# Kernel tuning notes

Hardware: AMD Instinct MI355X
Metric: run time of the kernel (lower is better)

Reference implementation:

```python
import jax, jax.numpy as jnp
import numpy as np

DIM = 1024
NUM_HEADS = 16
HEAD_DIM = DIM // NUM_HEADS
HIDDEN = 2 * DIM  # swiglu hidden


def rotate_half(x):
    x1, x2 = jnp.split(x, 2, axis=-1)
    return jnp.concatenate((-x2, x1), axis=-1)


def setup_inputs() -> dict:
    key = jax.random.key(0)
    ks = jax.random.split(key, 9)
    s = lambda fan_in: 1.0 / np.sqrt(fan_in)
    x = jax.random.normal(ks[0], (4, 2048, DIM), dtype=jnp.float32)
    qkv_w = jax.random.uniform(ks[1], (3 * DIM, DIM), minval=-s(DIM), maxval=s(DIM))
    proj_w = jax.random.uniform(ks[2], (DIM, DIM), minval=-s(DIM), maxval=s(DIM))
    proj_b = jax.random.uniform(ks[3], (DIM,), minval=-s(DIM), maxval=s(DIM))
    w1_w = jax.random.uniform(ks[4], (HIDDEN, DIM), minval=-s(DIM), maxval=s(DIM))
    w1_b = jnp.zeros((HIDDEN,), jnp.float32)
    w2_w = jax.random.uniform(ks[5], (HIDDEN, DIM), minval=-s(DIM), maxval=s(DIM))
    w2_b = jnp.zeros((HIDDEN,), jnp.float32)
    w3_w = jax.random.uniform(ks[6], (DIM, HIDDEN), minval=-s(HIDDEN), maxval=s(HIDDEN))
    w3_b = jnp.zeros((DIM,), jnp.float32)
    return {"x": x, "qkv_w": qkv_w, "proj_w": proj_w, "proj_b": proj_b,
            "w1_w": w1_w, "w1_b": w1_b, "w2_w": w2_w, "w2_b": w2_b,
            "w3_w": w3_w, "w3_b": w3_b}


def reference(x, qkv_w, proj_w, proj_b, w1_w, w1_b, w2_w, w2_b, w3_w, w3_b):
    B, N, C = x.shape
    H, D = NUM_HEADS, HEAD_DIM
    scale = D ** -0.5
    # QKV projection (no bias)
    qkv = jnp.einsum('bnc,fc->bnf', x, qkv_w).reshape(B, N, 3, H, D)
    qkv = jnp.transpose(qkv, (2, 0, 3, 1, 4))  # [3, B, H, N, D]
    q, k, v = qkv[0], qkv[1], qkv[2]
    # Rotary embeddings
    inv_freq = 1.0 / (10000.0 ** (jnp.arange(0, D, 2, dtype=jnp.float32) / D))
    t = jnp.arange(N, dtype=jnp.float32)
    freqs = jnp.einsum('i,j->ij', t, inv_freq)
    emb = jnp.concatenate((freqs, freqs), axis=-1)[None, None]  # [1,1,N,D]
    cos, sin = jnp.cos(emb), jnp.sin(emb)
    q = q * cos + rotate_half(q) * sin
    k = k * cos + rotate_half(k) * sin
    # Attention (non-causal, as in source)
    attn = jnp.einsum('bhnd,bhmd->bhnm', q, k) * scale
    attn = jax.nn.softmax(attn, axis=-1)
    out = jnp.einsum('bhnm,bhmd->bhnd', attn, v)
    out = jnp.transpose(out, (0, 2, 1, 3)).reshape(B, N, C)
    out = jnp.einsum('bnc,fc->bnf', out, proj_w) + proj_b
    # SwiGLU MLP
    x1 = jnp.einsum('bnc,fc->bnf', out, w1_w) + w1_b
    x2 = jnp.einsum('bnc,fc->bnf', out, w2_w) + w2_b
    hidden = jax.nn.silu(x1) * x2
    return jnp.einsum('bnh,fh->bnf', hidden, w3_w) + w3_b
```

## Files before the change

### kernel.cpp

```cpp
#include <hip/hip_runtime.h>
#include <hip/hip_bf16.h>
#include <math.h>


#define SEQ     2048
#define BATCH   4
#define NH      16
#define CDIM    1024
#define MROWS   8192

typedef __bf16 bf16x8 __attribute__((ext_vector_type(8)));
typedef float  floatx4 __attribute__((ext_vector_type(4)));
typedef float  floatx16 __attribute__((ext_vector_type(16)));
typedef unsigned int u32;

__device__ __forceinline__ unsigned short f2bf(float f) {
    __bf16 h = (__bf16)f;
    return __builtin_bit_cast(unsigned short, h);
}
__device__ __forceinline__ float fexp2(float x) {
    float r; asm("v_exp_f32 %0, %1" : "=v"(r) : "v"(x)); return r;
}
__device__ __forceinline__ float frcp(float x) {
    float r; asm("v_rcp_f32 %0, %1" : "=v"(r) : "v"(x)); return r;
}
__device__ __forceinline__ u32 cvtpk(float lo, float hi) {
    u32 w; asm("v_cvt_pk_bf16_f32 %0, %1, %2" : "=v"(w) : "v"(lo), "v"(hi));
    return w;
}
__device__ __forceinline__ floatx4 mfma16(bf16x8 a, bf16x8 b, floatx4 c) {
    return __builtin_amdgcn_mfma_f32_16x16x32_bf16(a, b, c, 0, 0, 0);
}
__device__ __forceinline__ floatx16 mfma32(bf16x8 a, bf16x8 b, floatx16 c) {
    return __builtin_amdgcn_mfma_f32_32x32x16_bf16(a, b, c, 0, 0, 0);
}
__device__ __forceinline__ void gld16(void* lds, const void* g) {
    __builtin_amdgcn_global_load_lds(
        (const __attribute__((address_space(1))) u32*)g,
        (__attribute__((address_space(3))) u32*)lds, 16, 0, 0);
}
__device__ __forceinline__ void wait_vm0_barrier() {
    asm volatile("s_waitcnt vmcnt(0)" ::: "memory");
    __builtin_amdgcn_s_barrier();
    __builtin_amdgcn_sched_barrier(0);
}
__device__ __forceinline__ void raw_barrier() {
    __builtin_amdgcn_s_barrier();
    __builtin_amdgcn_sched_barrier(0);
}

template <int OUTMODE, bool BIAS>
__global__ __launch_bounds__(256) void mgemm(
    const unsigned short* __restrict__ A,
    const unsigned short* __restrict__ B,
    const float* __restrict__ bias,
    void* __restrict__ C, int ldc,
    int K)
{
    __shared__ __align__(16) unsigned short As[2][128 * 32];
    __shared__ __align__(16) unsigned short Bs[2][128 * 32];

    const int tid  = threadIdx.x;
    const int lane = tid & 63;
    const int wave = tid >> 6;
    const int l16  = lane & 15;
    const int quad = lane >> 4;
    const int wm = (wave >> 1) * 64, wn = (wave & 1) * 64;
    const int bm = blockIdx.y, bn = blockIdx.x;

    const unsigned short* Ag = A + (size_t)(bm * 128) * K;
    const unsigned short* Bg = B + (size_t)(bn * 128) * K;

    const int srow0 = wave * 32 + (lane >> 2);
    const int scol  = 8 * ((lane & 3) ^ ((lane >> 3) & 3));
    const unsigned short* gA0 = Ag + (size_t)srow0 * K + scol;
    const unsigned short* gA1 = Ag + (size_t)(srow0 + 16) * K + scol;
    const unsigned short* gB0 = Bg + (size_t)srow0 * K + scol;
    const unsigned short* gB1 = Bg + (size_t)(srow0 + 16) * K + scol;

    auto stage = [&](int b, int kt) {
        gld16(&As[b][(wave * 2 + 0) * 512], gA0 + kt);
        gld16(&As[b][(wave * 2 + 1) * 512], gA1 + kt);
        gld16(&Bs[b][(wave * 2 + 0) * 512], gB0 + kt);
        gld16(&Bs[b][(wave * 2 + 1) * 512], gB1 + kt);
    };

    const int qsw = (quad ^ ((l16 >> 1) & 3)) * 8;

    floatx4 acc[4][4] = {};
    const int NK = K >> 5;

    stage(0, 0);
    wait_vm0_barrier();

    for (int i = 0; i < NK; ++i) {
        const int cur = i & 1;
        if (i + 1 < NK) stage(cur ^ 1, (i + 1) * 32);

        bf16x8 af[4], bfr[4];
        #pragma unroll
        for (int mt = 0; mt < 4; ++mt)
            af[mt] = *(const bf16x8*)&As[cur][(wm + mt * 16 + l16) * 32 + qsw];
        #pragma unroll
        for (int nt = 0; nt < 4; ++nt)
            bfr[nt] = *(const bf16x8*)&Bs[cur][(wn + nt * 16 + l16) * 32 + qsw];
        #pragma unroll
        for (int mt = 0; mt < 4; ++mt)
            #pragma unroll
            for (int nt = 0; nt < 4; ++nt)
                acc[mt][nt] = mfma16(af[mt], bfr[nt], acc[mt][nt]);

        if (i + 1 < NK) wait_vm0_barrier();
        else            raw_barrier();
    }

    #pragma unroll
    for (int nt = 0; nt < 4; ++nt) {
        const int gcol = bn * 128 + wn + nt * 16 + l16;
        const float bv = BIAS ? bias[gcol] : 0.0f;
        #pragma unroll
        for (int mt = 0; mt < 4; ++mt) {
            #pragma unroll
            for (int r = 0; r < 4; ++r) {
                const int grow = bm * 128 + wm + mt * 16 + quad * 4 + r;
                float v = acc[mt][nt][r] + bv;
                if (OUTMODE == 0)
                    ((float*)C)[(size_t)grow * ldc + gcol] = v;
                else
                    ((unsigned short*)C)[(size_t)grow * ldc + gcol] = f2bf(v);
            }
        }
    }
}

__global__ __launch_bounds__(256) void mgemm_glu(
    const unsigned short* __restrict__ A,
    const unsigned short* __restrict__ B1,
    const unsigned short* __restrict__ B2,
    const float* __restrict__ bias1,
    const float* __restrict__ bias2,
    unsigned short* __restrict__ C, int ldc,
    int K)
{
    __shared__ __align__(16) unsigned short As[2][128 * 32];
    __shared__ __align__(16) unsigned short B1s[2][64 * 32];
    __shared__ __align__(16) unsigned short B2s[2][64 * 32];

    const int tid  = threadIdx.x;
    const int lane = tid & 63;
    const int wave = tid >> 6;
    const int l16  = lane & 15;
    const int quad = lane >> 4;
    const int wm = (wave >> 1) * 64, wn = (wave & 1) * 32;
    const int bm = blockIdx.y, bn = blockIdx.x;

    const unsigned short* Ag  = A  + (size_t)(bm * 128) * K;
    const unsigned short* B1g = B1 + (size_t)(bn * 64) * K;
    const unsigned short* B2g = B2 + (size_t)(bn * 64) * K;

    const int arow = wave * 32 + (lane >> 2);
    const int brow = wave * 16 + (lane >> 2);
    const int scol = 8 * ((lane & 3) ^ ((lane >> 3) & 3));
    const unsigned short* gA0 = Ag  + (size_t)arow * K + scol;
    const unsigned short* gA1 = Ag  + (size_t)(arow + 16) * K + scol;
    const unsigned short* gB1 = B1g + (size_t)brow * K + scol;
    const unsigned short* gB2 = B2g + (size_t)brow * K + scol;

    auto stage = [&](int b, int kt) {
        gld16(&As[b][(wave * 2 + 0) * 512], gA0 + kt);
        gld16(&As[b][(wave * 2 + 1) * 512], gA1 + kt);
        gld16(&B1s[b][wave * 512], gB1 + kt);
        gld16(&B2s[b][wave * 512], gB2 + kt);
    };

    const int qsw = (quad ^ ((l16 >> 1) & 3)) * 8;

    floatx4 acc1[4][2] = {};
    floatx4 acc2[4][2] = {};
    const int NK = K >> 5;

    stage(0, 0);
    wait_vm0_barrier();

    for (int i = 0; i < NK; ++i) {
        const int cur = i & 1;
        if (i + 1 < NK) stage(cur ^ 1, (i + 1) * 32);

        bf16x8 af[4], b1f[2], b2f[2];
        #pragma unroll
        for (int mt = 0; mt < 4; ++mt)
            af[mt] = *(const bf16x8*)&As[cur][(wm + mt * 16 + l16) * 32 + qsw];
        #pragma unroll
        for (int nt = 0; nt < 2; ++nt) {
            b1f[nt] = *(const bf16x8*)&B1s[cur][(wn + nt * 16 + l16) * 32 + qsw];
            b2f[nt] = *(const bf16x8*)&B2s[cur][(wn + nt * 16 + l16) * 32 + qsw];
        }
        #pragma unroll
        for (int mt = 0; mt < 4; ++mt)
            #pragma unroll
            for (int nt = 0; nt < 2; ++nt) {
                acc1[mt][nt] = mfma16(af[mt], b1f[nt], acc1[mt][nt]);
                acc2[mt][nt] = mfma16(af[mt], b2f[nt], acc2[mt][nt]);
            }

        if (i + 1 < NK) wait_vm0_barrier();
        else            raw_barrier();
    }

    #pragma unroll
    for (int nt = 0; nt < 2; ++nt) {
        const int gcol = bn * 64 + wn + nt * 16 + l16;
        const float b1 = bias1[gcol];
        const float b2 = bias2[gcol];
        #pragma unroll
        for (int mt = 0; mt < 4; ++mt) {
            #pragma unroll
            for (int r = 0; r < 4; ++r) {
                const int grow = bm * 128 + wm + mt * 16 + quad * 4 + r;
                const float x1 = acc1[mt][nt][r] + b1;
                const float x2 = acc2[mt][nt][r] + b2;
                const float e = fexp2(x1 * -1.44269504088896f);
                const float v = x1 * frcp(1.0f + e) * x2;
                C[(size_t)grow * ldc + gcol] = f2bf(v);
            }
        }
    }
}

__global__ __launch_bounds__(256) void mgemm_qkv(
    const unsigned short* __restrict__ A,
    const unsigned short* __restrict__ B,
    const float* __restrict__ tab,
    unsigned short* __restrict__ Qb,
    unsigned short* __restrict__ Kb,
    unsigned short* __restrict__ Vtb)
{
    __shared__ __align__(16) unsigned short As[2][128 * 32];
    __shared__ __align__(16) unsigned short Bs[2][128 * 32];

    const int tid  = threadIdx.x;
    const int lane = tid & 63;
    const int wave = tid >> 6;
    const int l16  = lane & 15;
    const int quad = lane >> 4;
    const int wm = (wave >> 1) * 64, wn = (wave & 1) * 64;
    const int bm = blockIdx.y, bn = blockIdx.x;
    const int K = CDIM;

    const unsigned short* Ag = A + (size_t)(bm * 128) * K;
    const unsigned short* Bg = B + (size_t)(bn * 128) * K;

    const int srow0 = wave * 32 + (lane >> 2);
    const int scol  = 8 * ((lane & 3) ^ ((lane >> 3) & 3));
    const unsigned short* gA0 = Ag + (size_t)srow0 * K + scol;
    const unsigned short* gA1 = Ag + (size_t)(srow0 + 16) * K + scol;
    const unsigned short* gB0 = Bg + (size_t)srow0 * K + scol;
    const unsigned short* gB1 = Bg + (size_t)(srow0 + 16) * K + scol;

    auto stage = [&](int b, int kt) {
        gld16(&As[b][(wave * 2 + 0) * 512], gA0 + kt);
        gld16(&As[b][(wave * 2 + 1) * 512], gA1 + kt);
        gld16(&Bs[b][(wave * 2 + 0) * 512], gB0 + kt);
        gld16(&Bs[b][(wave * 2 + 1) * 512], gB1 + kt);
    };

    const int qsw = (quad ^ ((l16 >> 1) & 3)) * 8;

    floatx4 acc[4][4] = {};
    const int NK = K >> 5;

    stage(0, 0);
    wait_vm0_barrier();

    for (int i = 0; i < NK; ++i) {
        const int cur = i & 1;
        if (i + 1 < NK) stage(cur ^ 1, (i + 1) * 32);

        bf16x8 af[4], bfr[4];
        #pragma unroll
        for (int mt = 0; mt < 4; ++mt)
            af[mt] = *(const bf16x8*)&As[cur][(wm + mt * 16 + l16) * 32 + qsw];
        #pragma unroll
        for (int nt = 0; nt < 4; ++nt)
            bfr[nt] = *(const bf16x8*)&Bs[cur][(wn + nt * 16 + l16) * 32 + qsw];
        #pragma unroll
        for (int mt = 0; mt < 4; ++mt)
            #pragma unroll
            for (int nt = 0; nt < 4; ++nt)
                acc[mt][nt] = mfma16(af[mt], bfr[nt], acc[mt][nt]);

        if (i + 1 < NK) wait_vm0_barrier();
        else            raw_barrier();
    }

    const int colbase0 = bn * 128;
    const int part = colbase0 >> 10;

    if (part == 2) {
        unsigned short* T = &As[0][0];
        #pragma unroll
        for (int mt = 0; mt < 4; ++mt) {
            __syncthreads();
            #pragma unroll
            for (int nt = 0; nt < 4; ++nt) {
                ushort4 pk;
                pk.x = f2bf(acc[mt][nt][0]); pk.y = f2bf(acc[mt][nt][1]);
                pk.z = f2bf(acc[mt][nt][2]); pk.w = f2bf(acc[mt][nt][3]);
                *(ushort4*)&T[((wave * 64 + nt * 16 + l16) * 16) + quad * 4] = pk;
            }
            __syncthreads();
            const int w2 = tid >> 6, d = tid & 63;
            const int nrow0 = bm * 128 + (w2 >> 1) * 64 + mt * 16;
            const int b = nrow0 >> 11, n0 = nrow0 & 2047;
            const int h2 = ((bn * 128 + (w2 & 1) * 64) & 1023) >> 6;
            unsigned short* dst = Vtb +
                ((size_t)(b * NH + h2) * 64 + d) * 2048 + n0;
            const int tb = (w2 * 64 + d) * 16;
            *(uint4*)dst       = *(const uint4*)&T[tb];
            *(uint4*)(dst + 8) = *(const uint4*)&T[tb + 8];
        }
    } else {
        const float qscale = (part == 0) ? 0.125f * 1.44269504088896f : 1.0f;
        const int h = ((colbase0 + wn) & 1023) >> 6;
        #pragma unroll
        for (int mt = 0; mt < 4; ++mt) {
            #pragma unroll
            for (int r = 0; r < 4; ++r) {
                const int grow = bm * 128 + wm + mt * 16 + quad * 4 + r;
                const int b = grow >> 11, n = grow & 2047;
                unsigned short* dst =
                    (part == 0 ? Qb : Kb) + ((size_t)(b * NH + h) * 2048 + n) * 64;
                #pragma unroll
                for (int nt = 0; nt < 2; ++nt) {
                    const int i = nt * 16 + l16;
                    const float c  = tab[(n * 32 + i) * 2];
                    const float sn = tab[(n * 32 + i) * 2 + 1];
                    const float x1 = acc[mt][nt][r];
                    const float x2v = acc[mt][nt + 2][r];
                    dst[i]      = f2bf((x1 * c - x2v * sn) * qscale);
                    dst[i + 32] = f2bf((x2v * c + x1 * sn) * qscale);
                }
            }
        }
    }
}

__global__ __launch_bounds__(256) void attn_mfma(
    const unsigned short* __restrict__ Qb,
    const unsigned short* __restrict__ Kb,
    const unsigned short* __restrict__ Vtb,
    unsigned short* __restrict__ Ob)
{
    const int bh = blockIdx.x;
    const int qt = blockIdx.y;
    const int tid = threadIdx.x;
    const int lane = tid & 63, wave = tid >> 6;
    const int r32 = lane & 31, hi = lane >> 5;
    const int qrow = wave * 32 + r32;

    __shared__ unsigned short QP[128][72];
    __shared__ unsigned short Ks[64][72];
    __shared__ unsigned short Vs[64][72];

    const unsigned short* Qg = Qb + ((size_t)bh * 2048 + qt * 128) * 64;
    const unsigned short* Kg = Kb + (size_t)bh * 2048 * 64;
    const unsigned short* Vg = Vtb + (size_t)bh * 64 * 2048;

    #pragma unroll
    for (int rep = 0; rep < 4; ++rep) {
        const int c = tid + rep * 256;
        const int r = c >> 3, d0 = (c & 7) * 8;
        *(uint4*)&QP[r][d0] = *(const uint4*)(Qg + (size_t)r * 64 + d0);
    }

    const int c0 = tid, c1 = tid + 256;
    const int kr0 = c0 >> 3, kd0 = (c0 & 7) * 8;
    const int kr1 = c1 >> 3, kd1 = (c1 & 7) * 8;

    uint4 ka0 = *(const uint4*)(Kg + (size_t)kr0 * 64 + kd0);
    uint4 ka1 = *(const uint4*)(Kg + (size_t)kr1 * 64 + kd1);
    uint4 va0 = *(const uint4*)(Vg + (size_t)kr0 * 2048 + kd0);
    uint4 va1 = *(const uint4*)(Vg + (size_t)kr1 * 2048 + kd1);

    __syncthreads();

    bf16x8 bq[4];
    #pragma unroll
    for (int f = 0; f < 4; ++f)
        bq[f] = *(const bf16x8*)&QP[qrow][f * 16 + hi * 8];

    floatx16 o0 = {}, o1 = {};
    float l_acc = 0.0f;

    for (int kt = 0; kt < 32; ++kt) {
        __syncthreads();
        *(uint4*)&Ks[kr0][kd0] = ka0;
        *(uint4*)&Ks[kr1][kd1] = ka1;
        *(uint4*)&Vs[kr0][kd0] = va0;
        *(uint4*)&Vs[kr1][kd1] = va1;
        if (kt + 1 < 32) {
            const size_t nb = (size_t)(kt + 1) * 64;
            ka0 = *(const uint4*)(Kg + (nb + kr0) * 64 + kd0);
            ka1 = *(const uint4*)(Kg + (nb + kr1) * 64 + kd1);
            va0 = *(const uint4*)(Vg + (size_t)kr0 * 2048 + nb + kd0);
            va1 = *(const uint4*)(Vg + (size_t)kr1 * 2048 + nb + kd1);
        }
        __syncthreads();

        #pragma unroll
        for (int t = 0; t < 2; ++t) {
            floatx16 s = {};
            #pragma unroll
            for (int f = 0; f < 4; ++f) {
                const bf16x8 ak = *(const bf16x8*)&Ks[t * 32 + r32][f * 16 + hi * 8];
                s = mfma32(ak, bq[f], s);
            }
            float p[16];
            float rs = 0.0f;
            #pragma unroll
            for (int g = 0; g < 16; ++g) { p[g] = fexp2(s[g]); rs += p[g]; }
            l_acc += rs;
            u32 w0 = cvtpk(p[0], p[1]),   w2 = cvtpk(p[4], p[5]);
            u32 w1 = cvtpk(p[2], p[3]),   w3 = cvtpk(p[6], p[7]);
            u32 w4 = cvtpk(p[8], p[9]),   w6 = cvtpk(p[12], p[13]);
            u32 w5 = cvtpk(p[10], p[11]), w7 = cvtpk(p[14], p[15]);
            asm("v_permlane32_swap_b32 %0, %1" : "+v"(w0), "+v"(w2));
            asm("v_permlane32_swap_b32 %0, %1" : "+v"(w1), "+v"(w3));
            asm("v_permlane32_swap_b32 %0, %1" : "+v"(w4), "+v"(w6));
            asm("v_permlane32_swap_b32 %0, %1" : "+v"(w5), "+v"(w7));
            uint4 u0; u0.x = w0; u0.y = w1; u0.z = w2; u0.w = w3;
            uint4 u1; u1.x = w4; u1.y = w5; u1.z = w6; u1.w = w7;
            const bf16x8 bp0 = __builtin_bit_cast(bf16x8, u0);
            const bf16x8 bp1 = __builtin_bit_cast(bf16x8, u1);
            {
                const int f0 = 2 * t, f1 = 2 * t + 1;
                const bf16x8 av00 = *(const bf16x8*)&Vs[r32][f0 * 16 + hi * 8];
                const bf16x8 av01 = *(const bf16x8*)&Vs[32 + r32][f0 * 16 + hi * 8];
                o0 = mfma32(av00, bp0, o0);
                o1 = mfma32(av01, bp0, o1);
                const bf16x8 av10 = *(const bf16x8*)&Vs[r32][f1 * 16 + hi * 8];
                const bf16x8 av11 = *(const bf16x8*)&Vs[32 + r32][f1 * 16 + hi * 8];
                o0 = mfma32(av10, bp1, o0);
                o1 = mfma32(av11, bp1, o1);
            }
        }
    }

    const float l_tot = l_acc + __shfl_xor(l_acc, 32);
    const float inv = 1.0f / l_tot;
    const int b = bh >> 4, h = bh & 15;
    unsigned short* orow = Ob +
        (size_t)(b * SEQ + qt * 128 + qrow) * CDIM + h * 64;
    #pragma unroll
    for (int u = 0; u < 2; ++u) {
        const floatx16 ov = u ? o1 : o0;
        #pragma unroll
        for (int g = 0; g < 4; ++g) {
            ushort4 pk;
            pk.x = f2bf(ov[4 * g + 0] * inv); pk.y = f2bf(ov[4 * g + 1] * inv);
            pk.z = f2bf(ov[4 * g + 2] * inv); pk.w = f2bf(ov[4 * g + 3] * inv);
            *(ushort4*)(orow + u * 32 + 8 * g + 4 * hi) = pk;
        }
    }
}

__global__ __launch_bounds__(256) void cvt_all(
    const float* __restrict__ x,    const float* __restrict__ qkv,
    const float* __restrict__ proj, const float* __restrict__ w1,
    const float* __restrict__ w2,   const float* __restrict__ w3,
    unsigned short* __restrict__ xb,    unsigned short* __restrict__ qkvb,
    unsigned short* __restrict__ projb, unsigned short* __restrict__ w1b,
    unsigned short* __restrict__ w2b,   unsigned short* __restrict__ w3b)
{
    const size_t i = ((size_t)blockIdx.x * 256 + threadIdx.x) * 4;
    const float* src; unsigned short* dst; size_t off;
    if      (i <  8388608) { src = x;    dst = xb;    off = 0; }
    else if (i < 11534336) { src = qkv;  dst = qkvb;  off = 8388608; }
    else if (i < 12582912) { src = proj; dst = projb; off = 11534336; }
    else if (i < 14680064) { src = w1;   dst = w1b;   off = 12582912; }
    else if (i < 16777216) { src = w2;   dst = w2b;   off = 14680064; }
    else                   { src = w3;   dst = w3b;   off = 16777216; }
    const size_t j = i - off;
    const float4 f = *(const float4*)(src + j);
    ushort4 o; o.x = f2bf(f.x); o.y = f2bf(f.y); o.z = f2bf(f.z); o.w = f2bf(f.w);
    *(ushort4*)(dst + j) = o;
}

__global__ __launch_bounds__(256) void rope_table(float* __restrict__ tab)
{
    const int idx = blockIdx.x * 256 + threadIdx.x;
    const int i = idx & 31, n = idx >> 5;
    const double f = (double)n * pow(10000.0, -(double)(2 * i) / 64.0);
    tab[idx * 2]     = (float)cos(f);
    tab[idx * 2 + 1] = (float)sin(f);
}

extern "C" void kernel_launch(void* const* d_in, const int* in_sizes, int n_in,
                              void* d_out, int out_size, void* d_ws, size_t ws_size,
                              hipStream_t stream)
{
    const float* x      = (const float*)d_in[0];
    const float* qkv_w  = (const float*)d_in[1];
    const float* proj_w = (const float*)d_in[2];
    const float* proj_b = (const float*)d_in[3];
    const float* w1_w   = (const float*)d_in[4];
    const float* w1_b   = (const float*)d_in[5];
    const float* w2_w   = (const float*)d_in[6];
    const float* w2_b   = (const float*)d_in[7];
    const float* w3_w   = (const float*)d_in[8];
    const float* w3_b   = (const float*)d_in[9];
    float* out = (float*)d_out;

    char* ws = (char*)d_ws;
    unsigned short* Qb    = (unsigned short*)(ws);
    unsigned short* Kb    = (unsigned short*)(ws + 16777216);
    unsigned short* Vtb   = (unsigned short*)(ws + 33554432);
    unsigned short* Ob    = (unsigned short*)(ws + 50331648);
    unsigned short* out1b = (unsigned short*)(ws + 67108864);
    unsigned short* w1b   = (unsigned short*)(ws + 83886080);
    unsigned short* w2b   = (unsigned short*)(ws + 88080384);
    unsigned short* w3b   = (unsigned short*)(ws + 92274688);
    unsigned short* projb = (unsigned short*)(ws + 96468992);
    unsigned short* xb    = (unsigned short*)(ws + 98566144);
    unsigned short* wqkvb = (unsigned short*)(ws + 115343360);
    float*          tab   = (float*)(ws + 121634816);
    unsigned short* hid   = (unsigned short*)(ws);

    const dim3 blk(256);

    cvt_all<<<dim3(18432), blk, 0, stream>>>(
        x, qkv_w, proj_w, w1_w, w2_w, w3_w,
        xb, wqkvb, projb, w1b, w2b, w3b);
    rope_table<<<dim3(256), blk, 0, stream>>>(tab);

    mgemm_qkv<<<dim3(24, 64), blk, 0, stream>>>(xb, wqkvb, tab, Qb, Kb, Vtb);
    attn_mfma<<<dim3(BATCH * NH, SEQ / 128), blk, 0, stream>>>(Qb, Kb, Vtb, Ob);
    mgemm<1, true><<<dim3(8, 64), blk, 0, stream>>>(
        Ob, projb, proj_b, out1b, CDIM, CDIM);
    mgemm_glu<<<dim3(32, 64), blk, 0, stream>>>(
        out1b, w1b, w2b, w1_b, w2_b, hid, 2048, CDIM);
    mgemm<0, true><<<dim3(8, 64), blk, 0, stream>>>(
        hid, w3b, w3_b, out, CDIM, 2048);
}
```

Before: 475.0 us.

## Rewrite QKV GEMM as 256x256 tile, 8-wave ping-pong pipelined kernel

The QKV projection GEMM moves from 128x128 tiles with 4 waves and K-step 32 to 256x256 tiles with 8 waves and K-step 64. Loads are split into half-tile stages interleaved with MFMA phases, using explicit barriers, vmcnt waits, sched_barrier and setprio to overlap global loads with matrix math. The goal is more data reuse per byte loaded and better overlap of memory and compute. In exchange it uses far more LDS (128KB) and registers, and launches only 384 blocks, which may leave CUs underfilled.

```diff
diff --git a/kernel.cpp b/kernel.cpp
--- a/kernel.cpp
+++ b/kernel.cpp
@@ -227,7 +227,36 @@
     }
 }
 
-__global__ __launch_bounds__(256) void mgemm_qkv(
+#define RD_A(buf, mh)                                                     \
+    { _Pragma("unroll") for (int i_ = 0; i_ < 4; ++i_) {                  \
+        const int ro_ = (arow + ((mh) * 4 + i_) * 16) * 64;               \
+        aF[i_][0] = *(const bf16x8*)&As[buf][ro_ + e0];                   \
+        aF[i_][1] = *(const bf16x8*)&As[buf][ro_ + e1]; } }
+
+#define RD_B(buf, nh)                                                     \
+    { _Pragma("unroll") for (int n_ = 0; n_ < 2; ++n_) {                  \
+        const int ro_ = (brow + ((nh) * 2 + n_) * 16) * 64;               \
+        bF[nh][n_][0] = *(const bf16x8*)&Bs[buf][ro_ + e0];               \
+        bF[nh][n_][1] = *(const bf16x8*)&Bs[buf][ro_ + e1]; } }
+
+#define DO_MFMA(mh, nh)                                                   \
+    { _Pragma("unroll") for (int i_ = 0; i_ < 4; ++i_)                    \
+      { _Pragma("unroll") for (int n_ = 0; n_ < 2; ++n_) {                \
+        acc[(mh)*4+i_][(nh)*2+n_] =                                       \
+            mfma16(aF[i_][0], bF[nh][n_][0], acc[(mh)*4+i_][(nh)*2+n_]);  \
+        acc[(mh)*4+i_][(nh)*2+n_] =                                       \
+            mfma16(aF[i_][1], bF[nh][n_][1], acc[(mh)*4+i_][(nh)*2+n_]);  \
+      } } }
+
+#define PH_ENTER()                                                        \
+    __builtin_amdgcn_s_barrier();                                         \
+    asm volatile("s_waitcnt lgkmcnt(0)" ::: "memory");                    \
+    __builtin_amdgcn_sched_barrier(0);                                    \
+    __builtin_amdgcn_s_setprio(1)
+
+#define PH_EXIT() __builtin_amdgcn_s_setprio(0)
+
+__global__ __launch_bounds__(512, 2) void mgemm_qkv(
     const unsigned short* __restrict__ A,
     const unsigned short* __restrict__ B,
     const float* __restrict__ tab,
@@ -235,108 +264,151 @@
     unsigned short* __restrict__ Kb,
     unsigned short* __restrict__ Vtb)
 {
-    __shared__ __align__(16) unsigned short As[2][128 * 32];
-    __shared__ __align__(16) unsigned short Bs[2][128 * 32];
+    __shared__ __align__(16) unsigned short As[2][256 * 64];
+    __shared__ __align__(16) unsigned short Bs[2][256 * 64];
 
     const int tid  = threadIdx.x;
     const int lane = tid & 63;
     const int wave = tid >> 6;
     const int l16  = lane & 15;
     const int quad = lane >> 4;
-    const int wm = (wave >> 1) * 64, wn = (wave & 1) * 64;
-    const int bm = blockIdx.y, bn = blockIdx.x;
+    const int wr   = wave >> 2;
+    const int wc   = wave & 3;
+    const int bn = blockIdx.x, bm = blockIdx.y;
     const int K = CDIM;
 
-    const unsigned short* Ag = A + (size_t)(bm * 128) * K;
-    const unsigned short* Bg = B + (size_t)(bn * 128) * K;
-
-    const int srow0 = wave * 32 + (lane >> 2);
-    const int scol  = 8 * ((lane & 3) ^ ((lane >> 3) & 3));
-    const unsigned short* gA0 = Ag + (size_t)srow0 * K + scol;
-    const unsigned short* gA1 = Ag + (size_t)(srow0 + 16) * K + scol;
-    const unsigned short* gB0 = Bg + (size_t)srow0 * K + scol;
-    const unsigned short* gB1 = Bg + (size_t)(srow0 + 16) * K + scol;
-
-    auto stage = [&](int b, int kt) {
-        gld16(&As[b][(wave * 2 + 0) * 512], gA0 + kt);
-        gld16(&As[b][(wave * 2 + 1) * 512], gA1 + kt);
-        gld16(&Bs[b][(wave * 2 + 0) * 512], gB0 + kt);
-        gld16(&Bs[b][(wave * 2 + 1) * 512], gB1 + kt);
+    const unsigned short* Ag = A + (size_t)(bm * 256) * K;
+    const unsigned short* Bg = B + (size_t)(bn * 256) * K;
+
+    const int srow  = lane >> 3;
+    const int sgcol = ((lane & 7) ^ srow) * 8;
+
+    auto stA = [&](int buf, int half, int kt) {
+        #pragma unroll
+        for (int s = 0; s < 2; ++s) {
+            const int rbase = half * 128 + (wave * 2 + s) * 8;
+            gld16(&As[buf][rbase * 64],
+                  Ag + (size_t)(rbase + srow) * K + kt + sgcol);
+        }
     };
-
-    const int qsw = (quad ^ ((l16 >> 1) & 3)) * 8;
-
-    floatx4 acc[4][4] = {};
-    const int NK = K >> 5;
-
-    stage(0, 0);
-    wait_vm0_barrier();
-
-    for (int i = 0; i < NK; ++i) {
-        const int cur = i & 1;
-        if (i + 1 < NK) stage(cur ^ 1, (i + 1) * 32);
-
-        bf16x8 af[4], bfr[4];
-        #pragma unroll
-        for (int mt = 0; mt < 4; ++mt)
-            af[mt] = *(const bf16x8*)&As[cur][(wm + mt * 16 + l16) * 32 + qsw];
-        #pragma unroll
-        for (int nt = 0; nt < 4; ++nt)
-            bfr[nt] = *(const bf16x8*)&Bs[cur][(wn + nt * 16 + l16) * 32 + qsw];
-        #pragma unroll
-        for (int mt = 0; mt < 4; ++mt)
-            #pragma unroll
-            for (int nt = 0; nt < 4; ++nt)
-                acc[mt][nt] = mfma16(af[mt], bfr[nt], acc[mt][nt]);
-
-        if (i + 1 < NK) wait_vm0_barrier();
-        else            raw_barrier();
-    }
-
-    const int colbase0 = bn * 128;
-    const int part = colbase0 >> 10;
+    auto stB = [&](int buf, int half, int kt) {
+        #pragma unroll
+        for (int s = 0; s < 2; ++s) {
+            const int rbase = half * 128 + (wave * 2 + s) * 8;
+            gld16(&Bs[buf][rbase * 64],
+                  Bg + (size_t)(rbase + srow) * K + kt + sgcol);
+        }
+    };
+
+    const int e0 = ((quad)     ^ (l16 & 7)) * 8;
+    const int e1 = ((quad + 4) ^ (l16 & 7)) * 8;
+    const int arow = wr * 128 + l16;
+    const int brow = wc * 64 + l16;
+
+    floatx4 acc[8][4] = {};
+    bf16x8 aF[4][2];
+    bf16x8 bF[2][2][2];
+
+    stA(0, 0, 0); stA(0, 1, 0); stB(0, 0, 0); stB(0, 1, 0);
+    stA(1, 0, 64);
+    asm volatile("s_waitcnt vmcnt(2)" ::: "memory");
+    __builtin_amdgcn_s_barrier();
+    __builtin_amdgcn_sched_barrier(0);
+
+    for (int j = 0; j < 8; ++j) {
+        const int k1 = (2 * j + 1) * 64;
+        const int k2 = (2 * j + 2) * 64;
+        const int k3 = (2 * j + 3) * 64;
+        const bool more = (j < 7);
+
+        RD_A(0, 0); RD_B(0, 0);
+        stA(1, 1, k1);
+        PH_ENTER(); DO_MFMA(0, 0); PH_EXIT();
+        __builtin_amdgcn_s_barrier();
+
+        RD_B(0, 1);
+        stB(1, 0, k1);
+        PH_ENTER(); DO_MFMA(0, 1); PH_EXIT();
+        __builtin_amdgcn_s_barrier();
+
+        RD_A(0, 1);
+        stB(1, 1, k1);
+        PH_ENTER(); DO_MFMA(1, 1); PH_EXIT();
+        __builtin_amdgcn_s_barrier();
+
+        if (more) stA(0, 0, k2);
+        PH_ENTER(); DO_MFMA(1, 0); PH_EXIT();
+        if (more) { asm volatile("s_waitcnt vmcnt(2)" ::: "memory"); }
+        else      { asm volatile("s_waitcnt vmcnt(0)" ::: "memory"); }
+        __builtin_amdgcn_s_barrier();
+
+        RD_A(1, 0); RD_B(1, 0);
+        if (more) stA(0, 1, k2);
+        PH_ENTER(); DO_MFMA(0, 0); PH_EXIT();
+        __builtin_amdgcn_s_barrier();
+
+        RD_B(1, 1);
+        if (more) stB(0, 0, k2);
+        PH_ENTER(); DO_MFMA(0, 1); PH_EXIT();
+        __builtin_amdgcn_s_barrier();
+
+        RD_A(1, 1);
+        if (more) stB(0, 1, k2);
+        PH_ENTER(); DO_MFMA(1, 1); PH_EXIT();
+        __builtin_amdgcn_s_barrier();
+
+        if (more) stA(1, 0, k3);
+        PH_ENTER(); DO_MFMA(1, 0); PH_EXIT();
+        if (more) {
+            asm volatile("s_waitcnt vmcnt(2)" ::: "memory");
+            __builtin_amdgcn_s_barrier();
+        }
+    }
+
+    const int part = bn >> 2;
 
     if (part == 2) {
         unsigned short* T = &As[0][0];
         #pragma unroll
-        for (int mt = 0; mt < 4; ++mt) {
+        for (int m = 0; m < 8; ++m) {
             __syncthreads();
             #pragma unroll
-            for (int nt = 0; nt < 4; ++nt) {
+            for (int n = 0; n < 4; ++n) {
                 ushort4 pk;
-                pk.x = f2bf(acc[mt][nt][0]); pk.y = f2bf(acc[mt][nt][1]);
-                pk.z = f2bf(acc[mt][nt][2]); pk.w = f2bf(acc[mt][nt][3]);
-                *(ushort4*)&T[((wave * 64 + nt * 16 + l16) * 16) + quad * 4] = pk;
+                pk.x = f2bf(acc[m][n][0]); pk.y = f2bf(acc[m][n][1]);
+                pk.z = f2bf(acc[m][n][2]); pk.w = f2bf(acc[m][n][3]);
+                *(ushort4*)&T[(wr * 256 + wc * 64 + n * 16 + l16) * 16 + quad * 4] = pk;
             }
             __syncthreads();
-            const int w2 = tid >> 6, d = tid & 63;
-            const int nrow0 = bm * 128 + (w2 >> 1) * 64 + mt * 16;
-            const int b = nrow0 >> 11, n0 = nrow0 & 2047;
-            const int h2 = ((bn * 128 + (w2 & 1) * 64) & 1023) >> 6;
+            const int wr2 = tid >> 8, col = tid & 255;
+            const int grow0 = bm * 256 + wr2 * 128 + m * 16;
+            const int b = grow0 >> 11, n0 = grow0 & 2047;
+            const int h2 = (bn & 3) * 4 + (col >> 6);
+            const int d  = col & 63;
             unsigned short* dst = Vtb +
                 ((size_t)(b * NH + h2) * 64 + d) * 2048 + n0;
-            const int tb = (w2 * 64 + d) * 16;
+            const int tb = (wr2 * 256 + col) * 16;
             *(uint4*)dst       = *(const uint4*)&T[tb];
             *(uint4*)(dst + 8) = *(const uint4*)&T[tb + 8];
         }
     } else {
         const float qscale = (part == 0) ? 0.125f * 1.44269504088896f : 1.0f;
-        const int h = ((colbase0 + wn) & 1023) >> 6;
-        #pragma unroll
-        for (int mt = 0; mt < 4; ++mt) {
+        const int h = (bn & 3) * 4 + wc;
+        unsigned short* qk = (part == 0) ? Qb : Kb;
+        #pragma unroll
+        for (int m = 0; m < 8; ++m) {
             #pragma unroll
             for (int r = 0; r < 4; ++r) {
-                const int grow = bm * 128 + wm + mt * 16 + quad * 4 + r;
+                const int grow = bm * 256 + wr * 128 + m * 16 + quad * 4 + r;
                 const int b = grow >> 11, n = grow & 2047;
-                unsigned short* dst =
-                    (part == 0 ? Qb : Kb) + ((size_t)(b * NH + h) * 2048 + n) * 64;
+                unsigned short* dst = qk + ((size_t)(b * NH + h) * 2048 + n) * 64;
                 #pragma unroll
                 for (int nt = 0; nt < 2; ++nt) {
                     const int i = nt * 16 + l16;
                     const float c  = tab[(n * 32 + i) * 2];
                     const float sn = tab[(n * 32 + i) * 2 + 1];
-                    const float x1 = acc[mt][nt][r];
-                    const float x2v = acc[mt][nt + 2][r];
+                    const float x1  = acc[m][nt][r];
+                    const float x2v = acc[m][nt + 2][r];
                     dst[i]      = f2bf((x1 * c - x2v * sn) * qscale);
                     dst[i + 32] = f2bf((x2v * c + x1 * sn) * qscale);
                 }
@@ -533,7 +605,7 @@
         xb, wqkvb, projb, w1b, w2b, w3b);
     rope_table<<<dim3(256), blk, 0, stream>>>(tab);
 
-    mgemm_qkv<<<dim3(24, 64), blk, 0, stream>>>(xb, wqkvb, tab, Qb, Kb, Vtb);
+    mgemm_qkv<<<dim3(12, 32), dim3(512), 0, stream>>>(xb, wqkvb, tab, Qb, Kb, Vtb);
     attn_mfma<<<dim3(BATCH * NH, SEQ / 128), blk, 0, stream>>>(Qb, Kb, Vtb, Ob);
     mgemm<1, true><<<dim3(8, 64), blk, 0, stream>>>(
         Ob, projb, proj_b, out1b, CDIM, CDIM);
```

After: 443.3 us. 6.7% less time.
